# Optimization experiments

Hardware: AMD Instinct MI355X
Metric: run time of the kernel (lower is better)

The kernel has to match this reference:

```python
import jax, jax.numpy as jnp
import numpy as np

N_NODES = 100000
N_EDGES = 1600000
D_IN = 128
D_HID = 128
N_CLASSES = 1
N_GRAPHS = 64


def setup_inputs() -> dict:
    key = jax.random.key(0)
    ks = jax.random.split(key, 12)
    h = jax.random.normal(ks[0], (N_NODES, D_IN), dtype=jnp.float32)
    src = jax.random.randint(ks[1], (N_EDGES,), 0, N_NODES, dtype=jnp.int32)
    dst = jax.random.randint(ks[2], (N_EDGES,), 0, N_NODES, dtype=jnp.int32)
    node2graph = jnp.sort(jax.random.randint(ks[3], (N_NODES,), 0, N_GRAPHS, dtype=jnp.int32))
    s = 1.0 / np.sqrt(D_HID)
    W1 = jax.random.normal(ks[4], (D_IN, D_HID), dtype=jnp.float32) * s
    b1 = jnp.zeros((D_HID,), jnp.float32)
    W2 = jax.random.normal(ks[5], (D_HID, D_HID), dtype=jnp.float32) * s
    b2 = jnp.zeros((D_HID,), jnp.float32)
    Wc1 = jax.random.normal(ks[6], (D_HID, D_HID), dtype=jnp.float32) * s
    bc1 = jnp.zeros((D_HID,), jnp.float32)
    Wc2 = jax.random.normal(ks[7], (D_HID, D_HID), dtype=jnp.float32) * s
    bc2 = jnp.zeros((D_HID,), jnp.float32)
    Wc3 = jax.random.normal(ks[8], (D_HID, N_CLASSES), dtype=jnp.float32) * s
    bc3 = jnp.zeros((N_CLASSES,), jnp.float32)
    return dict(h=h, src=src, dst=dst, node2graph=node2graph,
                W1=W1, b1=b1, W2=W2, b2=b2,
                Wc1=Wc1, bc1=bc1, Wc2=Wc2, bc2=bc2, Wc3=Wc3, bc3=bc3)


def _degree_norms(src, dst):
    ones = jnp.ones(src.shape[0], jnp.float32)
    out_deg = jax.ops.segment_sum(ones, src, num_segments=N_NODES)
    in_deg = jax.ops.segment_sum(ones, dst, num_segments=N_NODES)
    # DGL GraphConv norm='both': degree clamped to >= 1, then ^-0.5
    out_norm = jnp.clip(out_deg, 1.0, None) ** -0.5
    in_norm = jnp.clip(in_deg, 1.0, None) ** -0.5
    return out_norm, in_norm


def _graph_conv(h, src, dst, out_norm, in_norm, W, b):
    # symmetric norm: D_dst^{-1/2} * sum_{src->dst} (D_src^{-1/2} * h_src) then linear
    msg = (h * out_norm[:, None])[src]  # [E, D]
    agg = jax.ops.segment_sum(msg, dst, num_segments=N_NODES)
    agg = agg * in_norm[:, None]
    return agg @ W + b


def reference(h, src, dst, node2graph, W1, b1, W2, b2, Wc1, bc1, Wc2, bc2, Wc3, bc3):
    out_norm, in_norm = _degree_norms(src, dst)
    h1 = jax.nn.relu(_graph_conv(h, src, dst, out_norm, in_norm, W1, b1))
    h2 = jax.nn.relu(_graph_conv(h1, src, dst, out_norm, in_norm, W2, b2))
    # dgl.mean_nodes: per-graph mean over nodes
    sums = jax.ops.segment_sum(h2, node2graph, num_segments=N_GRAPHS)  # [G, D]
    counts = jax.ops.segment_sum(jnp.ones(N_NODES, jnp.float32), node2graph, num_segments=N_GRAPHS)
    hg = sums / jnp.clip(counts, 1.0, None)[:, None]
    x = jax.nn.relu(hg @ Wc1 + bc1)
    x = jax.nn.relu(x @ Wc2 + bc2)
    return x @ Wc3 + bc3
```

## Files before the change

kernel.cpp:

```cpp
#include <hip/hip_runtime.h>
#include <hip/hip_fp16.h>

#define NN 100000
#define NE 1600000
#define D 128
#define NG 64
#define BM 64
#define POOL_CHUNK 64
#define SCAN_CHUNK 1024
#define NB_SCAN ((NN + SCAN_CHUNK - 1) / SCAN_CHUNK)

#define NCHUNK 64
#define CH_E (NE / NCHUNK)
#define HP 16384
#define NPART 7
#define HSTRIDE (NPART * HP)

typedef _Float16 half8 __attribute__((ext_vector_type(8)));
typedef float f32x4 __attribute__((ext_vector_type(4)));

__device__ __forceinline__ int lower_bound_i(const int* a, int n, int key) {
  int lo = 0, hi = n;
  while (lo < hi) { int mid = (lo + hi) >> 1; if (a[mid] < key) lo = mid + 1; else hi = mid; }
  return lo;
}

__global__ __launch_bounds__(256) void k_hist(
    const int* __restrict__ src, const int* __restrict__ dst,
    int* __restrict__ H) {
  __shared__ int pk[HP];
  const int c = blockIdx.x, p = blockIdx.y, t = threadIdx.x;
  const int base = p * HP;
  for (int i = t; i < HP; i += 256) pk[i] = 0;
  __syncthreads();
  const int4* s4 = (const int4*)(src + c * CH_E);
  const int4* d4 = (const int4*)(dst + c * CH_E);
  const int n4 = CH_E / 4;
  for (int i = t; i < n4; i += 256) {
    int4 s = s4[i], d = d4[i];
    if ((unsigned)(d.x - base) < HP) atomicAdd(&pk[d.x - base], 1);
    if ((unsigned)(d.y - base) < HP) atomicAdd(&pk[d.y - base], 1);
    if ((unsigned)(d.z - base) < HP) atomicAdd(&pk[d.z - base], 1);
    if ((unsigned)(d.w - base) < HP) atomicAdd(&pk[d.w - base], 1);
    if ((unsigned)(s.x - base) < HP) atomicAdd(&pk[s.x - base], 65536);
    if ((unsigned)(s.y - base) < HP) atomicAdd(&pk[s.y - base], 65536);
    if ((unsigned)(s.z - base) < HP) atomicAdd(&pk[s.z - base], 65536);
    if ((unsigned)(s.w - base) < HP) atomicAdd(&pk[s.w - base], 65536);
  }
  __syncthreads();
  size_t rb = (size_t)c * HSTRIDE + base;
  for (int i = t; i < HP; i += 256) H[rb + i] = pk[i];
}

__global__ __launch_bounds__(256) void k_reduce(
    const int* __restrict__ H,
    int* __restrict__ ic, float* __restrict__ onrm, float* __restrict__ inrm) {
  int n = blockIdx.x * 256 + threadIdx.x;
  if (n >= NN) return;
  int si = 0, so = 0;
#pragma unroll 8
  for (int c = 0; c < NCHUNK; ++c) {
    unsigned v = (unsigned)H[(size_t)c * HSTRIDE + n];
    si += (int)(v & 0xffffu);
    so += (int)(v >> 16);
  }
  ic[n] = si;
  inrm[n] = 1.0f / sqrtf((float)max(si, 1));
  onrm[n] = 1.0f / sqrtf((float)max(so, 1));
}

__global__ __launch_bounds__(256) void k_scan_a(const int* __restrict__ cnt,
                                                int* __restrict__ bsum) {
  int b = blockIdx.x, t = threadIdx.x;
  int idx = b * SCAN_CHUNK + t * 4;
  int4 v = make_int4(0, 0, 0, 0);
  if (idx < NN) v = *(const int4*)(cnt + idx);
  int s = v.x + v.y + v.z + v.w;
#pragma unroll
  for (int o = 1; o < 64; o <<= 1) s += __shfl_xor(s, o);
  __shared__ int ws[4];
  if ((t & 63) == 0) ws[t >> 6] = s;
  __syncthreads();
  if (t == 0) bsum[b] = ws[0] + ws[1] + ws[2] + ws[3];
}

__global__ void k_scan_b(int* __restrict__ bsum, int* __restrict__ off) {
  __shared__ int s[128];
  int t = threadIdx.x;
  int v = (t < NB_SCAN) ? bsum[t] : 0;
  s[t] = v;
  __syncthreads();
  for (int o = 1; o < 128; o <<= 1) {
    int u = (t >= o) ? s[t - o] : 0;
    __syncthreads();
    s[t] += u;
    __syncthreads();
  }
  if (t < NB_SCAN) bsum[t] = s[t] - v;
  if (t == 0) off[NN] = NE;
}

__global__ __launch_bounds__(256) void k_scan_c(const int* __restrict__ cnt,
                                                const int* __restrict__ bsum,
                                                int* __restrict__ off) {
  int b = blockIdx.x, t = threadIdx.x;
  int idx = b * SCAN_CHUNK + t * 4;
  int4 v = make_int4(0, 0, 0, 0);
  if (idx < NN) v = *(const int4*)(cnt + idx);
  int lsum = v.x + v.y + v.z + v.w;
  int lane = t & 63, wid = t >> 6;
  int x = lsum;
#pragma unroll
  for (int o = 1; o < 64; o <<= 1) {
    int u = __shfl_up(x, o);
    if (lane >= o) x += u;
  }
  __shared__ int wsum[4];
  if (lane == 63) wsum[wid] = x;
  __syncthreads();
  int woff = 0;
  for (int i = 0; i < 4; ++i) woff += (i < wid) ? wsum[i] : 0;
  int excl = x - lsum + woff + bsum[b];
  if (idx < NN) {
    int4 o4;
    o4.x = excl;
    o4.y = excl + v.x;
    o4.z = o4.y + v.y;
    o4.w = o4.z + v.z;
    *(int4*)(off + idx) = o4;
  }
}

__global__ __launch_bounds__(256) void k_start(int* __restrict__ H,
                                               const int* __restrict__ off) {
  int n = blockIdx.x * 256 + threadIdx.x;
  if (n >= NN) return;
  int run = off[n];
#pragma unroll 8
  for (int c = 0; c < NCHUNK; ++c) {
    size_t idx = (size_t)c * HSTRIDE + n;
    int v = H[idx];
    H[idx] = run;
    run += (int)((unsigned)v & 0xffffu);
  }
}

__global__ __launch_bounds__(256) void k_fill2(
    const int* __restrict__ src, const int* __restrict__ dst,
    const int* __restrict__ H, int* __restrict__ csr) {
  __shared__ int cur[HP];
  const int c = blockIdx.x, p = blockIdx.y, t = threadIdx.x;
  const int base = p * HP;
  size_t rb = (size_t)c * HSTRIDE + base;
  for (int i = t; i < HP; i += 256) cur[i] = H[rb + i];
  __syncthreads();
  const int4* s4 = (const int4*)(src + c * CH_E);
  const int4* d4 = (const int4*)(dst + c * CH_E);
  const int n4 = CH_E / 4;
  for (int i = t; i < n4; i += 256) {
    int4 s = s4[i], d = d4[i];
    if ((unsigned)(d.x - base) < HP) { int pos = atomicAdd(&cur[d.x - base], 1); csr[pos] = s.x; }
    if ((unsigned)(d.y - base) < HP) { int pos = atomicAdd(&cur[d.y - base], 1); csr[pos] = s.y; }
    if ((unsigned)(d.z - base) < HP) { int pos = atomicAdd(&cur[d.z - base], 1); csr[pos] = s.z; }
    if ((unsigned)(d.w - base) < HP) { int pos = atomicAdd(&cur[d.w - base], 1); csr[pos] = s.w; }
  }
}

template <typename AT>
__global__ __launch_bounds__(256, 4) void k_matmul(
    const AT* __restrict__ A, const float* __restrict__ W,
    const float* __restrict__ rs, __half* __restrict__ C) {
  __shared__ _Float16 Wt[128 * 136];
  const int tid = threadIdx.x;
  const int lane = tid & 63, wv = tid >> 6;
  const int row0 = blockIdx.x * BM + wv * 16;
#pragma unroll
  for (int i = 0; i < 16; ++i) {
    int idx = tid + i * 256;
    int k = idx >> 5, c0 = (idx & 31) * 4;
    float4 w4 = *(const float4*)&W[(size_t)k * 128 + c0];
    int k8 = k >> 3, ko = k & 7;
#pragma unroll
    for (int j = 0; j < 4; ++j) {
      int c = c0 + j;
      int kidx = (((k8 ^ ((c >> 3) & 15)) << 3) | ko);
      float v = (j == 0) ? w4.x : (j == 1) ? w4.y : (j == 2) ? w4.z : w4.w;
      Wt[c * 136 + kidx] = (_Float16)v;
    }
  }
  const int arow = row0 + (lane & 15);
  const bool valid = arow < NN;
  const float sc = valid ? rs[arow] : 0.f;
  half8 afr[4];
#pragma unroll
  for (int s = 0; s < 4; ++s) {
    half8 a;
    if constexpr (sizeof(AT) == 4) {
      const float* ap = (const float*)A + (size_t)arow * D + (lane >> 4) * 8;
      float4 lo = make_float4(0.f, 0.f, 0.f, 0.f), hi = lo;
      if (valid) {
        lo = *(const float4*)(ap + s * 32);
        hi = *(const float4*)(ap + s * 32 + 4);
      }
      a[0] = (_Float16)(lo.x * sc); a[1] = (_Float16)(lo.y * sc);
      a[2] = (_Float16)(lo.z * sc); a[3] = (_Float16)(lo.w * sc);
      a[4] = (_Float16)(hi.x * sc); a[5] = (_Float16)(hi.y * sc);
      a[6] = (_Float16)(hi.z * sc); a[7] = (_Float16)(hi.w * sc);
    } else {
      const _Float16* ap = (const _Float16*)A + (size_t)arow * D + (lane >> 4) * 8;
      half8 raw = {};
      if (valid) raw = *(const half8*)(ap + s * 32);
#pragma unroll
      for (int j = 0; j < 8; ++j) a[j] = (_Float16)((float)raw[j] * sc);
    }
    afr[s] = a;
  }
  __syncthreads();
  f32x4 acc[8];
#pragma unroll
  for (int ct = 0; ct < 8; ++ct) acc[ct] = (f32x4){0.f, 0.f, 0.f, 0.f};
#pragma unroll
  for (int s = 0; s < 4; ++s) {
    const int k8 = s * 4 + (lane >> 4);
#pragma unroll
    for (int ct = 0; ct < 8; ++ct) {
      int c = ct * 16 + (lane & 15);
      int kidx = ((k8 ^ ((c >> 3) & 15)) << 3);
      half8 b = *(const half8*)&Wt[c * 136 + kidx];
      acc[ct] = __builtin_amdgcn_mfma_f32_16x16x32_f16(afr[s], b, acc[ct], 0, 0, 0);
    }
  }
  const int dcol = lane & 15;
  const int drow0 = row0 + (lane >> 4) * 4;
#pragma unroll
  for (int ct = 0; ct < 8; ++ct) {
#pragma unroll
    for (int r = 0; r < 4; ++r) {
      int row = drow0 + r;
      if (row < NN)
        C[(size_t)row * D + ct * 16 + dcol] = __float2half_rn(acc[ct][r]);
    }
  }
}

__global__ __launch_bounds__(256) void k_gather(
    const __half* __restrict__ t, const int* __restrict__ csr,
    const int* __restrict__ off, const float* __restrict__ inn,
    const float* __restrict__ bias, __half* __restrict__ outp) {
  int w = (blockIdx.x * blockDim.x + threadIdx.x) >> 6;
  int lane = threadIdx.x & 63;
  if (w >= NN) return;
  int lo = off[w], hi = off[w + 1];
  const int g = lane >> 4;
  const int li = lane & 15;
  const __half* tp = t + li * 8;
  float a0 = 0.f, a1 = 0.f, a2 = 0.f, a3 = 0.f;
  float a4 = 0.f, a5 = 0.f, a6 = 0.f, a7 = 0.f;
  int e = lo + g;
  for (; e + 4 < hi; e += 8) {
    int s0 = csr[e];
    int s1 = csr[e + 4];
    float4 r0 = *(const float4*)(tp + (size_t)s0 * D);
    float4 r1 = *(const float4*)(tp + (size_t)s1 * D);
    const __half2* h0 = (const __half2*)&r0;
    const __half2* h1 = (const __half2*)&r1;
    float2 f00 = __half22float2(h0[0]);
    float2 f01 = __half22float2(h0[1]);
    float2 f02 = __half22float2(h0[2]);
    float2 f03 = __half22float2(h0[3]);
    float2 f10 = __half22float2(h1[0]);
    float2 f11 = __half22float2(h1[1]);
    float2 f12 = __half22float2(h1[2]);
    float2 f13 = __half22float2(h1[3]);
    a0 += f00.x + f10.x; a1 += f00.y + f10.y;
    a2 += f01.x + f11.x; a3 += f01.y + f11.y;
    a4 += f02.x + f12.x; a5 += f02.y + f12.y;
    a6 += f03.x + f13.x; a7 += f03.y + f13.y;
  }
  if (e < hi) {
    int s0 = csr[e];
    float4 r0 = *(const float4*)(tp + (size_t)s0 * D);
    const __half2* h0 = (const __half2*)&r0;
    float2 f00 = __half22float2(h0[0]);
    float2 f01 = __half22float2(h0[1]);
    float2 f02 = __half22float2(h0[2]);
    float2 f03 = __half22float2(h0[3]);
    a0 += f00.x; a1 += f00.y; a2 += f01.x; a3 += f01.y;
    a4 += f02.x; a5 += f02.y; a6 += f03.x; a7 += f03.y;
  }
  a0 += __shfl_xor(a0, 16); a0 += __shfl_xor(a0, 32);
  a1 += __shfl_xor(a1, 16); a1 += __shfl_xor(a1, 32);
  a2 += __shfl_xor(a2, 16); a2 += __shfl_xor(a2, 32);
  a3 += __shfl_xor(a3, 16); a3 += __shfl_xor(a3, 32);
  a4 += __shfl_xor(a4, 16); a4 += __shfl_xor(a4, 32);
  a5 += __shfl_xor(a5, 16); a5 += __shfl_xor(a5, 32);
  a6 += __shfl_xor(a6, 16); a6 += __shfl_xor(a6, 32);
  a7 += __shfl_xor(a7, 16); a7 += __shfl_xor(a7, 32);
  if (lane < 16) {
    float nm = inn[w];
    float4 b0 = *(const float4*)(bias + li * 8);
    float4 b1 = *(const float4*)(bias + li * 8 + 4);
    float o0 = fmaxf(fmaf(nm, a0, b0.x), 0.f);
    float o1 = fmaxf(fmaf(nm, a1, b0.y), 0.f);
    float o2 = fmaxf(fmaf(nm, a2, b0.z), 0.f);
    float o3 = fmaxf(fmaf(nm, a3, b0.w), 0.f);
    float o4 = fmaxf(fmaf(nm, a4, b1.x), 0.f);
    float o5 = fmaxf(fmaf(nm, a5, b1.y), 0.f);
    float o6 = fmaxf(fmaf(nm, a6, b1.z), 0.f);
    float o7 = fmaxf(fmaf(nm, a7, b1.w), 0.f);
    uint4 u;
    u.x = (unsigned)__half_as_ushort(__float2half_rn(o0)) |
          ((unsigned)__half_as_ushort(__float2half_rn(o1)) << 16);
    u.y = (unsigned)__half_as_ushort(__float2half_rn(o2)) |
          ((unsigned)__half_as_ushort(__float2half_rn(o3)) << 16);
    u.z = (unsigned)__half_as_ushort(__float2half_rn(o4)) |
          ((unsigned)__half_as_ushort(__float2half_rn(o5)) << 16);
    u.w = (unsigned)__half_as_ushort(__float2half_rn(o6)) |
          ((unsigned)__half_as_ushort(__float2half_rn(o7)) << 16);
    *(uint4*)(outp + (size_t)w * D + li * 8) = u;
  }
}

__global__ __launch_bounds__(128) void k_pool_partial(
    const __half* __restrict__ h2, const int* __restrict__ n2g,
    float* __restrict__ sums) {
  int c = threadIdx.x;
  int n0 = blockIdx.x * POOL_CHUNK;
  int n1 = min(n0 + POOL_CHUNK, NN);
  if (n0 >= NN) return;
  int gcur = n2g[n0];
  float acc = 0.f;
  for (int n = n0; n < n1; ++n) {
    int g = n2g[n];
    if (g != gcur) {
      atomicAdd(&sums[gcur * D + c], acc);
      acc = 0.f;
      gcur = g;
    }
    acc += __half2float(h2[(size_t)n * D + c]);
  }
  atomicAdd(&sums[gcur * D + c], acc);
}

__global__ void k_mlp(const float* __restrict__ sums, const int* __restrict__ n2g,
                      const float* __restrict__ Wc1, const float* __restrict__ bc1,
                      const float* __restrict__ Wc2, const float* __restrict__ bc2,
                      const float* __restrict__ Wc3, const float* __restrict__ bc3,
                      float* __restrict__ out) {
  __shared__ float xin[128];
  __shared__ float x1[128];
  __shared__ float red[128];
  int g = blockIdx.x, j = threadIdx.x;
  int start = lower_bound_i(n2g, NN, g);
  int end = lower_bound_i(n2g, NN, g + 1);
  float inv = 1.0f / (float)max(end - start, 1);
  xin[j] = sums[g * D + j] * inv;
  __syncthreads();
  float s = bc1[j];
#pragma unroll 8
  for (int k = 0; k < 128; ++k) s = fmaf(xin[k], Wc1[k * D + j], s);
  x1[j] = fmaxf(s, 0.f);
  __syncthreads();
  float s2 = bc2[j];
#pragma unroll 8
  for (int k = 0; k < 128; ++k) s2 = fmaf(x1[k], Wc2[k * D + j], s2);
  float v2 = fmaxf(s2, 0.f);
  red[j] = v2 * Wc3[j];
  __syncthreads();
  for (int o = 64; o > 0; o >>= 1) {
    if (j < o) red[j] += red[j + o];
    __syncthreads();
  }
  if (j == 0) out[g] = red[0] + bc3[0];
}

extern "C" void kernel_launch(void* const* d_in, const int* in_sizes, int n_in,
                              void* d_out, int out_size, void* d_ws, size_t ws_size,
                              hipStream_t stream) {
  const float* h   = (const float*)d_in[0];
  const int* src   = (const int*)d_in[1];
  const int* dst   = (const int*)d_in[2];
  const int* n2g   = (const int*)d_in[3];
  const float* W1  = (const float*)d_in[4];
  const float* b1  = (const float*)d_in[5];
  const float* W2  = (const float*)d_in[6];
  const float* b2  = (const float*)d_in[7];
  const float* Wc1 = (const float*)d_in[8];
  const float* bc1 = (const float*)d_in[9];
  const float* Wc2 = (const float*)d_in[10];
  const float* bc2 = (const float*)d_in[11];
  const float* Wc3 = (const float*)d_in[12];
  const float* bc3 = (const float*)d_in[13];
  float* out = (float*)d_out;

  char* p = (char*)d_ws;
  size_t o = 0;
  auto take = [&](size_t b) { void* q = p + o; o = (o + b + 255) & ~(size_t)255; return q; };
  float* sums = (float*)take(NG * D * 4);
  size_t zero_bytes = o;
  int* off   = (int*)take((NN + 1) * 4);
  int* bsum  = (int*)take(NB_SCAN * 4);
  int* ic    = (int*)take(NN * 4);
  float* onrm = (float*)take(NN * 4);
  float* inrm = (float*)take(NN * 4);
  int* csr   = (int*)take((size_t)NE * 4);
  __half* tbuf = (__half*)take((size_t)NN * D * 2);
  __half* hbuf = (__half*)take((size_t)NN * D * 4);
  (void)ws_size; (void)in_sizes; (void)n_in; (void)out_size;

  int* H = (int*)hbuf;

  hipMemsetAsync(d_ws, 0, zero_bytes, stream);
  dim3 hgrid(NCHUNK, NPART);
  k_hist<<<hgrid, 256, 0, stream>>>(src, dst, H);
  k_reduce<<<(NN + 255) / 256, 256, 0, stream>>>(H, ic, onrm, inrm);
  k_scan_a<<<NB_SCAN, 256, 0, stream>>>(ic, bsum);
  k_scan_b<<<1, 128, 0, stream>>>(bsum, off);
  k_scan_c<<<NB_SCAN, 256, 0, stream>>>(ic, bsum, off);
  k_start<<<(NN + 255) / 256, 256, 0, stream>>>(H, off);
  k_fill2<<<hgrid, 256, 0, stream>>>(src, dst, H, csr);

  k_matmul<float><<<(NN + BM - 1) / BM, 256, 0, stream>>>(h, W1, onrm, tbuf);
  k_gather<<<(NN * 64) / 256, 256, 0, stream>>>(tbuf, csr, off, inrm, b1, hbuf);
  k_matmul<__half><<<(NN + BM - 1) / BM, 256, 0, stream>>>(hbuf, W2, onrm, tbuf);
  k_gather<<<(NN * 64) / 256, 256, 0, stream>>>(tbuf, csr, off, inrm, b2, hbuf);

  k_pool_partial<<<(NN + POOL_CHUNK - 1) / POOL_CHUNK, 128, 0, stream>>>(hbuf, n2g, sums);
  k_mlp<<<NG, 128, 0, stream>>>(sums, n2g, Wc1, bc1, Wc2, bc2, Wc3, bc3, out);
}
```

Baseline: 272.5 us.

## Store features in column-sliced layout so each gather wave reads one 16-column slice

Node feature buffers switch from row-major [N,128] to eight column slices of [N,16] fp16. The matmul writes and reads them in this layout, and the pooling kernel reads them the same way. The gather kernel now gives each block one slice for four destination nodes, and each lane reads 8 bytes per edge. The aim is a smaller working set per slice (about 3.2 MB), so random neighbour reads hit cache better. In exchange, each edge's index is read eight times, each gather is much smaller, and the launch has many more blocks with longer shuffle reductions.

```diff
diff --git a/kernel.cpp b/kernel.cpp
--- a/kernel.cpp
+++ b/kernel.cpp
@@ -9,6 +9,7 @@
 #define POOL_CHUNK 64
 #define SCAN_CHUNK 1024
 #define NB_SCAN ((NN + SCAN_CHUNK - 1) / SCAN_CHUNK)
+#define PS ((size_t)NN * 16)
 
 #define NCHUNK 64
 #define CH_E (NE / NCHUNK)
@@ -207,9 +208,11 @@
       a[4] = (_Float16)(hi.x * sc); a[5] = (_Float16)(hi.y * sc);
       a[6] = (_Float16)(hi.z * sc); a[7] = (_Float16)(hi.w * sc);
     } else {
-      const _Float16* ap = (const _Float16*)A + (size_t)arow * D + (lane >> 4) * 8;
+      int j0 = s * 32 + (lane >> 4) * 8;
+      const _Float16* ap = (const _Float16*)A + (size_t)(j0 >> 4) * PS +
+                           (size_t)arow * 16 + (j0 & 15);
       half8 raw = {};
-      if (valid) raw = *(const half8*)(ap + s * 32);
+      if (valid) raw = *(const half8*)ap;
 #pragma unroll
       for (int j = 0; j < 8; ++j) a[j] = (_Float16)((float)raw[j] * sc);
     }
@@ -238,7 +241,7 @@
     for (int r = 0; r < 4; ++r) {
       int row = drow0 + r;
       if (row < NN)
-        C[(size_t)row * D + ct * 16 + dcol] = __float2half_rn(acc[ct][r]);
+        C[(size_t)ct * PS + (size_t)row * 16 + dcol] = __float2half_rn(acc[ct][r]);
     }
   }
 }
@@ -247,77 +250,42 @@
     const __half* __restrict__ t, const int* __restrict__ csr,
     const int* __restrict__ off, const float* __restrict__ inn,
     const float* __restrict__ bias, __half* __restrict__ outp) {
-  int w = (blockIdx.x * blockDim.x + threadIdx.x) >> 6;
-  int lane = threadIdx.x & 63;
+  const int slice = blockIdx.x & 7;
+  const int wgrp = blockIdx.x >> 3;
+  const int wv = threadIdx.x >> 6;
+  const int w = wgrp * 4 + wv;
+  const int lane = threadIdx.x & 63;
   if (w >= NN) return;
   int lo = off[w], hi = off[w + 1];
-  const int g = lane >> 4;
-  const int li = lane & 15;
-  const __half* tp = t + li * 8;
+  const int g = lane >> 2;
+  const int li = lane & 3;
+  const __half* tp = t + (size_t)slice * PS + li * 4;
   float a0 = 0.f, a1 = 0.f, a2 = 0.f, a3 = 0.f;
-  float a4 = 0.f, a5 = 0.f, a6 = 0.f, a7 = 0.f;
-  int e = lo + g;
-  for (; e + 4 < hi; e += 8) {
-    int s0 = csr[e];
-    int s1 = csr[e + 4];
-    float4 r0 = *(const float4*)(tp + (size_t)s0 * D);
-    float4 r1 = *(const float4*)(tp + (size_t)s1 * D);
-    const __half2* h0 = (const __half2*)&r0;
-    const __half2* h1 = (const __half2*)&r1;
-    float2 f00 = __half22float2(h0[0]);
-    float2 f01 = __half22float2(h0[1]);
-    float2 f02 = __half22float2(h0[2]);
-    float2 f03 = __half22float2(h0[3]);
-    float2 f10 = __half22float2(h1[0]);
-    float2 f11 = __half22float2(h1[1]);
-    float2 f12 = __half22float2(h1[2]);
-    float2 f13 = __half22float2(h1[3]);
-    a0 += f00.x + f10.x; a1 += f00.y + f10.y;
-    a2 += f01.x + f11.x; a3 += f01.y + f11.y;
-    a4 += f02.x + f12.x; a5 += f02.y + f12.y;
-    a6 += f03.x + f13.x; a7 += f03.y + f13.y;
-  }
-  if (e < hi) {
-    int s0 = csr[e];
-    float4 r0 = *(const float4*)(tp + (size_t)s0 * D);
-    const __half2* h0 = (const __half2*)&r0;
-    float2 f00 = __half22float2(h0[0]);
-    float2 f01 = __half22float2(h0[1]);
-    float2 f02 = __half22float2(h0[2]);
-    float2 f03 = __half22float2(h0[3]);
-    a0 += f00.x; a1 += f00.y; a2 += f01.x; a3 += f01.y;
-    a4 += f02.x; a5 += f02.y; a6 += f03.x; a7 += f03.y;
-  }
-  a0 += __shfl_xor(a0, 16); a0 += __shfl_xor(a0, 32);
-  a1 += __shfl_xor(a1, 16); a1 += __shfl_xor(a1, 32);
-  a2 += __shfl_xor(a2, 16); a2 += __shfl_xor(a2, 32);
-  a3 += __shfl_xor(a3, 16); a3 += __shfl_xor(a3, 32);
-  a4 += __shfl_xor(a4, 16); a4 += __shfl_xor(a4, 32);
-  a5 += __shfl_xor(a5, 16); a5 += __shfl_xor(a5, 32);
-  a6 += __shfl_xor(a6, 16); a6 += __shfl_xor(a6, 32);
-  a7 += __shfl_xor(a7, 16); a7 += __shfl_xor(a7, 32);
-  if (lane < 16) {
+  for (int e = lo + g; e < hi; e += 16) {
+    int s = csr[e];
+    float2 raw = *(const float2*)(tp + (size_t)s * 16);
+    const __half2* hp = (const __half2*)&raw;
+    float2 f0 = __half22float2(hp[0]);
+    float2 f1 = __half22float2(hp[1]);
+    a0 += f0.x; a1 += f0.y; a2 += f1.x; a3 += f1.y;
+  }
+  a0 += __shfl_xor(a0, 4); a0 += __shfl_xor(a0, 8); a0 += __shfl_xor(a0, 16); a0 += __shfl_xor(a0, 32);
+  a1 += __shfl_xor(a1, 4); a1 += __shfl_xor(a1, 8); a1 += __shfl_xor(a1, 16); a1 += __shfl_xor(a1, 32);
+  a2 += __shfl_xor(a2, 4); a2 += __shfl_xor(a2, 8); a2 += __shfl_xor(a2, 16); a2 += __shfl_xor(a2, 32);
+  a3 += __shfl_xor(a3, 4); a3 += __shfl_xor(a3, 8); a3 += __shfl_xor(a3, 16); a3 += __shfl_xor(a3, 32);
+  if (lane < 4) {
     float nm = inn[w];
-    float4 b0 = *(const float4*)(bias + li * 8);
-    float4 b1 = *(const float4*)(bias + li * 8 + 4);
-    float o0 = fmaxf(fmaf(nm, a0, b0.x), 0.f);
-    float o1 = fmaxf(fmaf(nm, a1, b0.y), 0.f);
-    float o2 = fmaxf(fmaf(nm, a2, b0.z), 0.f);
-    float o3 = fmaxf(fmaf(nm, a3, b0.w), 0.f);
-    float o4 = fmaxf(fmaf(nm, a4, b1.x), 0.f);
-    float o5 = fmaxf(fmaf(nm, a5, b1.y), 0.f);
-    float o6 = fmaxf(fmaf(nm, a6, b1.z), 0.f);
-    float o7 = fmaxf(fmaf(nm, a7, b1.w), 0.f);
-    uint4 u;
+    float4 b4 = *(const float4*)(bias + slice * 16 + li * 4);
+    float o0 = fmaxf(fmaf(nm, a0, b4.x), 0.f);
+    float o1 = fmaxf(fmaf(nm, a1, b4.y), 0.f);
+    float o2 = fmaxf(fmaf(nm, a2, b4.z), 0.f);
+    float o3 = fmaxf(fmaf(nm, a3, b4.w), 0.f);
+    uint2 u;
     u.x = (unsigned)__half_as_ushort(__float2half_rn(o0)) |
           ((unsigned)__half_as_ushort(__float2half_rn(o1)) << 16);
     u.y = (unsigned)__half_as_ushort(__float2half_rn(o2)) |
           ((unsigned)__half_as_ushort(__float2half_rn(o3)) << 16);
-    u.z = (unsigned)__half_as_ushort(__float2half_rn(o4)) |
-          ((unsigned)__half_as_ushort(__float2half_rn(o5)) << 16);
-    u.w = (unsigned)__half_as_ushort(__float2half_rn(o6)) |
-          ((unsigned)__half_as_ushort(__float2half_rn(o7)) << 16);
-    *(uint4*)(outp + (size_t)w * D + li * 8) = u;
+    *(uint2*)(outp + (size_t)slice * PS + (size_t)w * 16 + li * 4) = u;
   }
 }
 
@@ -328,6 +296,7 @@
   int n0 = blockIdx.x * POOL_CHUNK;
   int n1 = min(n0 + POOL_CHUNK, NN);
   if (n0 >= NN) return;
+  const __half* hp = h2 + (size_t)(c >> 4) * PS + (c & 15);
   int gcur = n2g[n0];
   float acc = 0.f;
   for (int n = n0; n < n1; ++n) {
@@ -337,7 +306,7 @@
       acc = 0.f;
       gcur = g;
     }
-    acc += __half2float(h2[(size_t)n * D + c]);
+    acc += __half2float(hp[(size_t)n * 16]);
   }
   atomicAdd(&sums[gcur * D + c], acc);
 }
@@ -418,12 +387,14 @@
   k_scan_b<<<1, 128, 0, stream>>>(bsum, off);
   k_scan_c<<<NB_SCAN, 256, 0, stream>>>(ic, bsum, off);
   k_start<<<(NN + 255) / 256, 256, 0, stream>>>(H, off);
-  k_fill2<<<hgrid, 256, 0, stream>>>(src, dst, H, csr);
-
+  dim3 fgrid(NCHUNK, NPART);
+  k_fill2<<<fgrid, 256, 0, stream>>>(src, dst, H, csr);
+
+  const int gblocks = ((NN + 3) / 4) * 8;
   k_matmul<float><<<(NN + BM - 1) / BM, 256, 0, stream>>>(h, W1, onrm, tbuf);
-  k_gather<<<(NN * 64) / 256, 256, 0, stream>>>(tbuf, csr, off, inrm, b1, hbuf);
+  k_gather<<<gblocks, 256, 0, stream>>>(tbuf, csr, off, inrm, b1, hbuf);
   k_matmul<__half><<<(NN + BM - 1) / BM, 256, 0, stream>>>(hbuf, W2, onrm, tbuf);
-  k_gather<<<(NN * 64) / 256, 256, 0, stream>>>(tbuf, csr, off, inrm, b2, hbuf);
+  k_gather<<<gblocks, 256, 0, stream>>>(tbuf, csr, off, inrm, b2, hbuf);
 
   k_pool_partial<<<(NN + POOL_CHUNK - 1) / POOL_CHUNK, 128, 0, stream>>>(hbuf, n2g, sums);
   k_mlp<<<NG, 128, 0, stream>>>(sums, n2g, Wc1, bc1, Wc2, bc2, Wc3, bc3, out);
```

Result: slower. 553.1 us (+102.9%).
